# Performance work log

Measured on AMD Instinct MI355X. Metric: run time of the kernel, lower is better.

## Reference

```python
import jax, jax.numpy as jnp
import numpy as np

NUM_EXPERTS = 8


def setup_inputs() -> dict:
    key = jax.random.key(0)
    k1, k2, k3, k4 = jax.random.split(key, 4)
    T, H, I, E = 1024, 1024, 4096, NUM_EXPERTS
    return {
        "hidden_states": jax.random.normal(k1, (T, H), dtype=jnp.float32),
        "w1": jax.random.normal(k2, (E, 2 * I, H), dtype=jnp.float32) * 0.02,
        "w2": jax.random.normal(k3, (E, H, I), dtype=jnp.float32) * 0.02,
        "gating_output": jax.random.normal(k4, (T, E), dtype=jnp.float32),
        "topk": 2,
    }


def reference(hidden_states, w1, w2, gating_output, topk):
    # Faithful single-device version of jax_fused_moe_func (renormalize=True,
    # reduce_results=True). The original sorts token copies by expert id and runs
    # a grouped matmul (megablox gmm), then reverts the sort; mathematically each
    # token copy is multiplied by its expert's weights, which we compute directly
    # (no sort/unsort permutation needed since it cancels).
    orig_shape = hidden_states.shape
    dtype = hidden_states.dtype
    H = hidden_states.shape[-1]
    T = hidden_states.size // H
    E = w1.shape[0]
    I = w2.shape[-1]  # intermediate_size

    hs = hidden_states.reshape(T, H)
    gates = gating_output.reshape(T, E)

    probs = jax.nn.softmax(gates.astype(jnp.float32), axis=-1)
    topk_weights, topk_indices = jax.lax.top_k(probs, k=topk)
    topk_weights = topk_weights / topk_weights.sum(axis=-1, keepdims=True)  # renormalize
    topk_weights = topk_weights.astype(dtype)

    flat_ids = topk_indices.reshape(-1)            # [T*topk] expert id per token copy
    x = jnp.repeat(hs, topk, axis=0)               # [T*topk, H] token copies

    out = jnp.zeros((T * topk, H), dtype=dtype)
    for e in range(E):  # fixed small expert loop (emulates grouped GEMM)
        h = x @ w1[e].T                            # [m, 2I]
        act = jax.nn.silu(h[:, :I]) * h[:, I:]     # SwiGLU
        y = act @ w2[e].T                          # [m, H]
        out = jnp.where((flat_ids == e)[:, None], y, out)

    out = (out.reshape(T, topk, H) * topk_weights[..., None]).sum(axis=-2)
    return out.reshape(orig_shape)
```

## Files before the change

kernel.cpp:

```cpp
#include <hip/hip_runtime.h>

#define T_TOK 1024
#define H_DIM 1024
#define I_DIM 4096
#define NE 8

typedef __attribute__((ext_vector_type(8))) short bf16x8;
typedef __attribute__((ext_vector_type(4))) float f32x4;
typedef __attribute__((ext_vector_type(8))) unsigned short us8;
typedef __attribute__((ext_vector_type(4))) short s16x4;

__device__ __forceinline__ unsigned short f2bf(float x) {
  union { float f; unsigned u; } v; v.f = x;
  unsigned r = v.u + 0x7fffu + ((v.u >> 16) & 1u);
  return (unsigned short)(r >> 16);
}

__global__ void k_route(const float* __restrict__ gates, int* __restrict__ counts,
                        int* __restrict__ tok_idx, float* __restrict__ tok_w) {
  int t = blockIdx.x * blockDim.x + threadIdx.x;
  if (t >= T_TOK) return;
  float g[NE];
#pragma unroll
  for (int e = 0; e < NE; ++e) g[e] = gates[t * NE + e];
  int i1 = 0; float g1 = g[0];
#pragma unroll
  for (int e = 1; e < NE; ++e) if (g[e] > g1) { g1 = g[e]; i1 = e; }
  int i2 = -1; float g2 = -1e30f;
#pragma unroll
  for (int e = 0; e < NE; ++e) if (e != i1 && g[e] > g2) { g2 = g[e]; i2 = e; }
  float wa = 1.0f / (1.0f + expf(g2 - g1));
  float wb = 1.0f - wa;
  int s1 = atomicAdd(&counts[i1], 1);
  tok_idx[i1 * T_TOK + s1] = t;
  tok_w[i1 * T_TOK + s1] = wa;
  int s2 = atomicAdd(&counts[i2], 1);
  tok_idx[i2 * T_TOK + s2] = t;
  tok_w[i2 * T_TOK + s2] = wb;
}

__global__ void k_pack(const float* __restrict__ hs, const int* __restrict__ counts,
                       const int* __restrict__ tok_idx, const float* __restrict__ tok_w,
                       unsigned short* __restrict__ xpack, int* __restrict__ row_tok,
                       float* __restrict__ row_w) {
  int e = blockIdx.x >> 10, slot = blockIdx.x & 1023;
  if (slot >= counts[e]) return;
  int off = 0;
#pragma unroll
  for (int i = 0; i < NE; ++i) if (i < e) off += counts[i];
  int row = off + slot;
  int tok = tok_idx[e * T_TOK + slot];
  if (threadIdx.x == 0) { row_tok[row] = tok; row_w[row] = tok_w[e * T_TOK + slot]; }
  float4 v = ((const float4*)(hs + (size_t)tok * H_DIM))[threadIdx.x];
  ushort4 o = make_ushort4(f2bf(v.x), f2bf(v.y), f2bf(v.z), f2bf(v.w));
  ((ushort4*)(xpack + (size_t)row * H_DIM))[threadIdx.x] = o;
}

#define BM 64
#define BK 64

__global__ __launch_bounds__(256, 2)
void k_gemm1(const float* __restrict__ w1, const unsigned short* __restrict__ xpack,
             const int* __restrict__ counts, unsigned short* __restrict__ act) {
  int b = blockIdx.x;
  int p = ((b >> 7) << 3) | (b & 7);
  int mtile = (b >> 3) & 15;
  int e = p >> 6;
  int ntile = p & 63;
  int cnt = counts[e];
  int m0 = mtile * BM;
  if (m0 >= cnt) return;
  int off = 0;
#pragma unroll
  for (int i = 0; i < NE; ++i) if (i < e) off += counts[i];
  int n0 = ntile * 64;

  __shared__ __align__(16) short As[BM * BK];
  __shared__ __align__(16) short Bs[128 * BK];

  int tid = threadIdx.x;
  int lane = tid & 63, wid = tid >> 6;
  int wm = wid & 1, wn = wid >> 1;
  int lr = lane & 15, lk8 = (lane >> 4) * 8;

  const float* w1e = w1 + (size_t)e * (2 * I_DIM) * H_DIM;
  const unsigned short* xb = xpack + (size_t)(off + m0) * H_DIM;

  int arow0 = tid >> 3, ack = tid & 7;
  int brow0 = tid >> 4, bck = tid & 15;

  f32x4 acc[2][4];
#pragma unroll
  for (int i = 0; i < 2; ++i)
#pragma unroll
    for (int j = 0; j < 4; ++j) acc[i][j] = (f32x4){0.f, 0.f, 0.f, 0.f};

  us8 aReg[2];
  float4 bReg[8];

  auto loadA = [&](int k0) {
#pragma unroll
    for (int i = 0; i < 2; ++i) {
      int r = arow0 + i * 32;
      us8 z = {0, 0, 0, 0, 0, 0, 0, 0};
      aReg[i] = (m0 + r < cnt) ? *(const us8*)(xb + (size_t)r * H_DIM + k0 + ack * 8) : z;
    }
  };
  auto loadB = [&](int k0) {
#pragma unroll
    for (int i = 0; i < 8; ++i) {
      int r = brow0 + i * 16;
      int grow = ((r & 16) ? I_DIM : 0) + n0 + ((r >> 5) << 4) + (r & 15);
      bReg[i] = *(const float4*)(w1e + (size_t)grow * H_DIM + k0 + bck * 4);
    }
  };

  loadA(0); loadB(0);

  for (int ks = 0; ks < H_DIM / BK; ++ks) {
    __syncthreads();
#pragma unroll
    for (int i = 0; i < 2; ++i) {
      int r = arow0 + i * 32;
      *(us8*)&As[r * BK + ((ack * 8) ^ ((r & 7) << 3))] = aReg[i];
    }
#pragma unroll
    for (int i = 0; i < 8; ++i) {
      int r = brow0 + i * 16;
      float4 v = bReg[i];
      s16x4 sv = {(short)f2bf(v.x), (short)f2bf(v.y), (short)f2bf(v.z), (short)f2bf(v.w)};
      *(s16x4*)&Bs[r * BK + ((bck * 4) ^ ((r & 7) << 3))] = sv;
    }
    __syncthreads();
    if (ks + 1 < H_DIM / BK) { loadA((ks + 1) * BK); loadB((ks + 1) * BK); }
#pragma unroll
    for (int kk = 0; kk < 2; ++kk) {
      int k0 = kk * 32 + lk8;
      bf16x8 a[2], bb[4];
#pragma unroll
      for (int mr = 0; mr < 2; ++mr) {
        int r = wm * 32 + mr * 16 + lr;
        a[mr] = *(const bf16x8*)&As[r * BK + (k0 ^ ((r & 7) << 3))];
      }
#pragma unroll
      for (int nr = 0; nr < 4; ++nr) {
        int r = (wn * 4 + nr) * 16 + lr;
        bb[nr] = *(const bf16x8*)&Bs[r * BK + (k0 ^ ((r & 7) << 3))];
      }
#pragma unroll
      for (int mr = 0; mr < 2; ++mr)
#pragma unroll
        for (int nr = 0; nr < 4; ++nr)
          acc[mr][nr] = __builtin_amdgcn_mfma_f32_16x16x32_bf16(a[mr], bb[nr], acc[mr][nr], 0, 0, 0);
    }
  }

#pragma unroll
  for (int mr = 0; mr < 2; ++mr) {
#pragma unroll
    for (int pp = 0; pp < 2; ++pp) {
      f32x4 g = acc[mr][2 * pp], u = acc[mr][2 * pp + 1];
      int ncol = n0 + (wn * 2 + pp) * 16 + lr;
#pragma unroll
      for (int q = 0; q < 4; ++q) {
        int rl = wm * 32 + mr * 16 + (lane >> 4) * 4 + q;
        if (m0 + rl < cnt) {
          float gv = g[q];
          float av = gv / (1.0f + expf(-gv)) * u[q];
          act[(size_t)(off + m0 + rl) * I_DIM + ncol] = f2bf(av);
        }
      }
    }
  }
}

__global__ __launch_bounds__(256, 2)
void k_gemm2(const float* __restrict__ w2, const unsigned short* __restrict__ act,
             const int* __restrict__ counts, const int* __restrict__ row_tok,
             const float* __restrict__ row_w, float* __restrict__ out) {
  int b = blockIdx.x;
  int p = ((b >> 7) << 3) | (b & 7);
  int mtile = (b >> 3) & 15;
  int e = p >> 3;
  int ntile = p & 7;
  int cnt = counts[e];
  int m0 = mtile * BM;
  if (m0 >= cnt) return;
  int off = 0;
#pragma unroll
  for (int i = 0; i < NE; ++i) if (i < e) off += counts[i];
  int n0 = ntile * 128;

  __shared__ __align__(16) short As[BM * BK];
  __shared__ __align__(16) short Bs[128 * BK];

  int tid = threadIdx.x;
  int lane = tid & 63, wid = tid >> 6;
  int wm = wid & 1, wn = wid >> 1;
  int lr = lane & 15, lk8 = (lane >> 4) * 8;

  const float* w2e = w2 + (size_t)e * H_DIM * I_DIM;
  const unsigned short* ab = act + (size_t)(off + m0) * I_DIM;

  int arow0 = tid >> 3, ack = tid & 7;
  int brow0 = tid >> 4, bck = tid & 15;

  f32x4 acc[2][4];
#pragma unroll
  for (int i = 0; i < 2; ++i)
#pragma unroll
    for (int j = 0; j < 4; ++j) acc[i][j] = (f32x4){0.f, 0.f, 0.f, 0.f};

  us8 aReg[2];
  float4 bReg[8];

  auto loadA = [&](int k0) {
#pragma unroll
    for (int i = 0; i < 2; ++i) {
      int r = arow0 + i * 32;
      us8 z = {0, 0, 0, 0, 0, 0, 0, 0};
      aReg[i] = (m0 + r < cnt) ? *(const us8*)(ab + (size_t)r * I_DIM + k0 + ack * 8) : z;
    }
  };
  auto loadB = [&](int k0) {
#pragma unroll
    for (int i = 0; i < 8; ++i) {
      int r = brow0 + i * 16;
      bReg[i] = *(const float4*)(w2e + (size_t)(n0 + r) * I_DIM + k0 + bck * 4);
    }
  };

  loadA(0); loadB(0);

  for (int ks = 0; ks < I_DIM / BK; ++ks) {
    __syncthreads();
#pragma unroll
    for (int i = 0; i < 2; ++i) {
      int r = arow0 + i * 32;
      *(us8*)&As[r * BK + ((ack * 8) ^ ((r & 7) << 3))] = aReg[i];
    }
#pragma unroll
    for (int i = 0; i < 8; ++i) {
      int r = brow0 + i * 16;
      float4 v = bReg[i];
      s16x4 sv = {(short)f2bf(v.x), (short)f2bf(v.y), (short)f2bf(v.z), (short)f2bf(v.w)};
      *(s16x4*)&Bs[r * BK + ((bck * 4) ^ ((r & 7) << 3))] = sv;
    }
    __syncthreads();
    if (ks + 1 < I_DIM / BK) { loadA((ks + 1) * BK); loadB((ks + 1) * BK); }
#pragma unroll
    for (int kk = 0; kk < 2; ++kk) {
      int k0 = kk * 32 + lk8;
      bf16x8 a[2], bb[4];
#pragma unroll
      for (int mr = 0; mr < 2; ++mr) {
        int r = wm * 32 + mr * 16 + lr;
        a[mr] = *(const bf16x8*)&As[r * BK + (k0 ^ ((r & 7) << 3))];
      }
#pragma unroll
      for (int nr = 0; nr < 4; ++nr) {
        int r = (wn * 4 + nr) * 16 + lr;
        bb[nr] = *(const bf16x8*)&Bs[r * BK + (k0 ^ ((r & 7) << 3))];
      }
#pragma unroll
      for (int mr = 0; mr < 2; ++mr)
#pragma unroll
        for (int nr = 0; nr < 4; ++nr)
          acc[mr][nr] = __builtin_amdgcn_mfma_f32_16x16x32_bf16(a[mr], bb[nr], acc[mr][nr], 0, 0, 0);
    }
  }

#pragma unroll
  for (int mr = 0; mr < 2; ++mr) {
#pragma unroll
    for (int q = 0; q < 4; ++q) {
      int rl = wm * 32 + mr * 16 + (lane >> 4) * 4 + q;
      if (m0 + rl >= cnt) continue;
      int grow = off + m0 + rl;
      float wgt = row_w[grow];
      float* orow = out + (size_t)row_tok[grow] * H_DIM;
#pragma unroll
      for (int nr = 0; nr < 4; ++nr) {
        int ncol = n0 + (wn * 4 + nr) * 16 + lr;
        atomicAdd(&orow[ncol], acc[mr][nr][q] * wgt);
      }
    }
  }
}

extern "C" void kernel_launch(void* const* d_in, const int* in_sizes, int n_in,
                              void* d_out, int out_size, void* d_ws, size_t ws_size,
                              hipStream_t stream) {
  const float* hs = (const float*)d_in[0];
  const float* w1 = (const float*)d_in[1];
  const float* w2 = (const float*)d_in[2];
  const float* gates = (const float*)d_in[3];
  float* out = (float*)d_out;

  char* ws = (char*)d_ws;
  int* counts = (int*)ws;
  int* tok_idx = (int*)(ws + 1024);
  float* tok_w = (float*)(ws + 1024 + 32768);
  int* row_tok = (int*)(ws + 1024 + 65536);
  float* row_w = (float*)(ws + 1024 + 65536 + 8192);
  unsigned short* xpack = (unsigned short*)(ws + 131072);
  unsigned short* act = (unsigned short*)(ws + 131072 + 2048 * 1024 * 2);

  hipMemsetAsync(counts, 0, NE * sizeof(int), stream);
  hipMemsetAsync(d_out, 0, (size_t)out_size * sizeof(float), stream);
  k_route<<<dim3(4), dim3(256), 0, stream>>>(gates, counts, tok_idx, tok_w);
  k_pack<<<dim3(NE * T_TOK), dim3(256), 0, stream>>>(hs, counts, tok_idx, tok_w, xpack, row_tok, row_w);
  k_gemm1<<<dim3(8192), dim3(256), 0, stream>>>(w1, xpack, counts, act);
  k_gemm2<<<dim3(1024), dim3(256), 0, stream>>>(w2, act, counts, row_tok, row_w, out);
}
```

Baseline: 268.9 us.

## Enlarge gemm1 M-tile to 128 and replace gemm2 atomics with combine kernel

The gate/up GEMM now uses 128-row M tiles with a 4x4 MFMA accumulator per wave. This halves the number of blocks and the number of times each expert weight panel is re-read and converted from fp32. The down GEMM writes weighted per-row results into a scratch buffer instead of issuing atomicAdds into the output. A new combine kernel then sums each token's two copies through an inverse row map built in the pack step, which also removes the output memset. The price is more registers per thread in gemm1, extra scratch traffic for y, and one more kernel launch.

```diff
diff --git a/kernel.cpp b/kernel.cpp
--- a/kernel.cpp
+++ b/kernel.cpp
@@ -17,7 +17,8 @@
 }
 
 __global__ void k_route(const float* __restrict__ gates, int* __restrict__ counts,
-                        int* __restrict__ tok_idx, float* __restrict__ tok_w) {
+                        int* __restrict__ tok_idx, float* __restrict__ tok_w,
+                        int* __restrict__ tok_cpy) {
   int t = blockIdx.x * blockDim.x + threadIdx.x;
   if (t >= T_TOK) return;
   float g[NE];
@@ -32,17 +33,16 @@
   float wa = 1.0f / (1.0f + expf(g2 - g1));
   float wb = 1.0f - wa;
   int s1 = atomicAdd(&counts[i1], 1);
-  tok_idx[i1 * T_TOK + s1] = t;
-  tok_w[i1 * T_TOK + s1] = wa;
+  tok_idx[i1 * T_TOK + s1] = t; tok_w[i1 * T_TOK + s1] = wa; tok_cpy[i1 * T_TOK + s1] = 0;
   int s2 = atomicAdd(&counts[i2], 1);
-  tok_idx[i2 * T_TOK + s2] = t;
-  tok_w[i2 * T_TOK + s2] = wb;
+  tok_idx[i2 * T_TOK + s2] = t; tok_w[i2 * T_TOK + s2] = wb; tok_cpy[i2 * T_TOK + s2] = 1;
 }
 
 __global__ void k_pack(const float* __restrict__ hs, const int* __restrict__ counts,
                        const int* __restrict__ tok_idx, const float* __restrict__ tok_w,
-                       unsigned short* __restrict__ xpack, int* __restrict__ row_tok,
-                       float* __restrict__ row_w) {
+                       const int* __restrict__ tok_cpy, unsigned short* __restrict__ xpack,
+                       int* __restrict__ row_tok, float* __restrict__ row_w,
+                       int* __restrict__ inv_row) {
   int e = blockIdx.x >> 10, slot = blockIdx.x & 1023;
   if (slot >= counts[e]) return;
   int off = 0;
@@ -50,32 +50,35 @@
   for (int i = 0; i < NE; ++i) if (i < e) off += counts[i];
   int row = off + slot;
   int tok = tok_idx[e * T_TOK + slot];
-  if (threadIdx.x == 0) { row_tok[row] = tok; row_w[row] = tok_w[e * T_TOK + slot]; }
+  if (threadIdx.x == 0) {
+    row_tok[row] = tok;
+    row_w[row] = tok_w[e * T_TOK + slot];
+    inv_row[tok * 2 + tok_cpy[e * T_TOK + slot]] = row;
+  }
   float4 v = ((const float4*)(hs + (size_t)tok * H_DIM))[threadIdx.x];
   ushort4 o = make_ushort4(f2bf(v.x), f2bf(v.y), f2bf(v.z), f2bf(v.w));
   ((ushort4*)(xpack + (size_t)row * H_DIM))[threadIdx.x] = o;
 }
 
-#define BM 64
 #define BK 64
 
 __global__ __launch_bounds__(256, 2)
 void k_gemm1(const float* __restrict__ w1, const unsigned short* __restrict__ xpack,
              const int* __restrict__ counts, unsigned short* __restrict__ act) {
   int b = blockIdx.x;
-  int p = ((b >> 7) << 3) | (b & 7);
-  int mtile = (b >> 3) & 15;
-  int e = p >> 6;
-  int ntile = p & 63;
+  int x = b & 7, s = b >> 3;
+  int mt = s & 7, pl = s >> 3;
+  int panel = pl * 8 + x;
+  int e = panel >> 6, ntile = panel & 63;
   int cnt = counts[e];
-  int m0 = mtile * BM;
+  int m0 = mt * 128;
   if (m0 >= cnt) return;
   int off = 0;
 #pragma unroll
   for (int i = 0; i < NE; ++i) if (i < e) off += counts[i];
   int n0 = ntile * 64;
 
-  __shared__ __align__(16) short As[BM * BK];
+  __shared__ __align__(16) short As[128 * BK];
   __shared__ __align__(16) short Bs[128 * BK];
 
   int tid = threadIdx.x;
@@ -89,18 +92,18 @@
   int arow0 = tid >> 3, ack = tid & 7;
   int brow0 = tid >> 4, bck = tid & 15;
 
-  f32x4 acc[2][4];
-#pragma unroll
-  for (int i = 0; i < 2; ++i)
+  f32x4 acc[4][4];
+#pragma unroll
+  for (int i = 0; i < 4; ++i)
 #pragma unroll
     for (int j = 0; j < 4; ++j) acc[i][j] = (f32x4){0.f, 0.f, 0.f, 0.f};
 
-  us8 aReg[2];
+  us8 aReg[4];
   float4 bReg[8];
 
   auto loadA = [&](int k0) {
 #pragma unroll
-    for (int i = 0; i < 2; ++i) {
+    for (int i = 0; i < 4; ++i) {
       int r = arow0 + i * 32;
       us8 z = {0, 0, 0, 0, 0, 0, 0, 0};
       aReg[i] = (m0 + r < cnt) ? *(const us8*)(xb + (size_t)r * H_DIM + k0 + ack * 8) : z;
@@ -120,7 +123,7 @@
   for (int ks = 0; ks < H_DIM / BK; ++ks) {
     __syncthreads();
 #pragma unroll
-    for (int i = 0; i < 2; ++i) {
+    for (int i = 0; i < 4; ++i) {
       int r = arow0 + i * 32;
       *(us8*)&As[r * BK + ((ack * 8) ^ ((r & 7) << 3))] = aReg[i];
     }
@@ -136,19 +139,19 @@
 #pragma unroll
     for (int kk = 0; kk < 2; ++kk) {
       int k0 = kk * 32 + lk8;
-      bf16x8 a[2], bb[4];
-#pragma unroll
-      for (int mr = 0; mr < 2; ++mr) {
-        int r = wm * 32 + mr * 16 + lr;
+      bf16x8 a[4], bb[4];
+#pragma unroll
+      for (int mr = 0; mr < 4; ++mr) {
+        int r = wm * 64 + mr * 16 + lr;
         a[mr] = *(const bf16x8*)&As[r * BK + (k0 ^ ((r & 7) << 3))];
       }
 #pragma unroll
       for (int nr = 0; nr < 4; ++nr) {
-        int r = (wn * 4 + nr) * 16 + lr;
+        int r = wn * 64 + nr * 16 + lr;
         bb[nr] = *(const bf16x8*)&Bs[r * BK + (k0 ^ ((r & 7) << 3))];
       }
 #pragma unroll
-      for (int mr = 0; mr < 2; ++mr)
+      for (int mr = 0; mr < 4; ++mr)
 #pragma unroll
         for (int nr = 0; nr < 4; ++nr)
           acc[mr][nr] = __builtin_amdgcn_mfma_f32_16x16x32_bf16(a[mr], bb[nr], acc[mr][nr], 0, 0, 0);
@@ -156,14 +159,14 @@
   }
 
 #pragma unroll
-  for (int mr = 0; mr < 2; ++mr) {
+  for (int mr = 0; mr < 4; ++mr) {
 #pragma unroll
     for (int pp = 0; pp < 2; ++pp) {
       f32x4 g = acc[mr][2 * pp], u = acc[mr][2 * pp + 1];
       int ncol = n0 + (wn * 2 + pp) * 16 + lr;
 #pragma unroll
       for (int q = 0; q < 4; ++q) {
-        int rl = wm * 32 + mr * 16 + (lane >> 4) * 4 + q;
+        int rl = wm * 64 + mr * 16 + (lane >> 4) * 4 + q;
         if (m0 + rl < cnt) {
           float gv = g[q];
           float av = gv / (1.0f + expf(-gv)) * u[q];
@@ -176,22 +179,21 @@
 
 __global__ __launch_bounds__(256, 2)
 void k_gemm2(const float* __restrict__ w2, const unsigned short* __restrict__ act,
-             const int* __restrict__ counts, const int* __restrict__ row_tok,
-             const float* __restrict__ row_w, float* __restrict__ out) {
+             const int* __restrict__ counts, const float* __restrict__ row_w,
+             float* __restrict__ y) {
   int b = blockIdx.x;
-  int p = ((b >> 7) << 3) | (b & 7);
-  int mtile = (b >> 3) & 15;
-  int e = p >> 3;
-  int ntile = p & 7;
+  int x = b & 7, s = b >> 3;
+  int mt = s & 15, e = s >> 4;
+  int ntile = x;
   int cnt = counts[e];
-  int m0 = mtile * BM;
+  int m0 = mt * 64;
   if (m0 >= cnt) return;
   int off = 0;
 #pragma unroll
   for (int i = 0; i < NE; ++i) if (i < e) off += counts[i];
   int n0 = ntile * 128;
 
-  __shared__ __align__(16) short As[BM * BK];
+  __shared__ __align__(16) short As[64 * BK];
   __shared__ __align__(16) short Bs[128 * BK];
 
   int tid = threadIdx.x;
@@ -278,14 +280,24 @@
       if (m0 + rl >= cnt) continue;
       int grow = off + m0 + rl;
       float wgt = row_w[grow];
-      float* orow = out + (size_t)row_tok[grow] * H_DIM;
+      float* yrow = y + (size_t)grow * H_DIM;
 #pragma unroll
       for (int nr = 0; nr < 4; ++nr) {
         int ncol = n0 + (wn * 4 + nr) * 16 + lr;
-        atomicAdd(&orow[ncol], acc[mr][nr][q] * wgt);
-      }
-    }
-  }
+        yrow[ncol] = acc[mr][nr][q] * wgt;
+      }
+    }
+  }
+}
+
+__global__ void k_combine(const float* __restrict__ y, const int* __restrict__ inv_row,
+                          float* __restrict__ out) {
+  int t = blockIdx.x, i = threadIdx.x;
+  const float4* ya = (const float4*)(y + (size_t)inv_row[2 * t] * H_DIM);
+  const float4* yb = (const float4*)(y + (size_t)inv_row[2 * t + 1] * H_DIM);
+  float4 a = ya[i], b2 = yb[i];
+  ((float4*)(out + (size_t)t * H_DIM))[i] =
+      make_float4(a.x + b2.x, a.y + b2.y, a.z + b2.z, a.w + b2.w);
 }
 
 extern "C" void kernel_launch(void* const* d_in, const int* in_sizes, int n_in,
@@ -299,17 +311,21 @@
 
   char* ws = (char*)d_ws;
   int* counts = (int*)ws;
-  int* tok_idx = (int*)(ws + 1024);
-  float* tok_w = (float*)(ws + 1024 + 32768);
-  int* row_tok = (int*)(ws + 1024 + 65536);
-  float* row_w = (float*)(ws + 1024 + 65536 + 8192);
-  unsigned short* xpack = (unsigned short*)(ws + 131072);
-  unsigned short* act = (unsigned short*)(ws + 131072 + 2048 * 1024 * 2);
+  int* tok_idx = (int*)(ws + 4096);
+  float* tok_w = (float*)(ws + 4096 + 32768);
+  int* tok_cpy = (int*)(ws + 4096 + 65536);
+  int* row_tok = (int*)(ws + 4096 + 98304);
+  float* row_w = (float*)(ws + 4096 + 98304 + 8192);
+  int* inv_row = (int*)(ws + 4096 + 98304 + 16384);
+  unsigned short* xpack = (unsigned short*)(ws + (1 << 17));
+  unsigned short* act = (unsigned short*)(ws + (8u << 20));
+  float* y = (float*)(ws + (32u << 20));
 
   hipMemsetAsync(counts, 0, NE * sizeof(int), stream);
-  hipMemsetAsync(d_out, 0, (size_t)out_size * sizeof(float), stream);
-  k_route<<<dim3(4), dim3(256), 0, stream>>>(gates, counts, tok_idx, tok_w);
-  k_pack<<<dim3(NE * T_TOK), dim3(256), 0, stream>>>(hs, counts, tok_idx, tok_w, xpack, row_tok, row_w);
-  k_gemm1<<<dim3(8192), dim3(256), 0, stream>>>(w1, xpack, counts, act);
-  k_gemm2<<<dim3(1024), dim3(256), 0, stream>>>(w2, act, counts, row_tok, row_w, out);
-}
+  k_route<<<dim3(4), dim3(256), 0, stream>>>(gates, counts, tok_idx, tok_w, tok_cpy);
+  k_pack<<<dim3(NE * T_TOK), dim3(256), 0, stream>>>(hs, counts, tok_idx, tok_w, tok_cpy,
+                                                     xpack, row_tok, row_w, inv_row);
+  k_gemm1<<<dim3(4096), dim3(256), 0, stream>>>(w1, xpack, counts, act);
+  k_gemm2<<<dim3(1024), dim3(256), 0, stream>>>(w2, act, counts, row_w, y);
+  k_combine<<<dim3(T_TOK), dim3(256), 0, stream>>>(y, inv_row, out);
+}
```

Result: slower. 280.6 us (+4.4%).
